# Kernel tuning notes

Hardware: AMD Instinct MI355X
Metric: run time of the kernel (lower is better)

The kernel has to match this reference:

```python
import jax, jax.numpy as jnp
import numpy as np

B, S, D = 4, 2048, 2048  # batch, seq, input_dim == state_dim
N = D

def setup_inputs() -> dict:
    key = jax.random.key(0)
    ks = jax.random.split(key, 6)
    x = jax.random.normal(ks[0], (B, S, D), dtype=jnp.float32)
    W_dt = jax.random.normal(ks[1], (N, D), dtype=jnp.float32) / np.sqrt(D)
    b_dt = jnp.ones((N,), dtype=jnp.float32)  # dt_proj.bias.fill_(1.0)
    W_B = jax.random.normal(ks[2], (N, D), dtype=jnp.float32) / np.sqrt(D)
    W_C = jax.random.normal(ks[3], (D, N), dtype=jnp.float32) / np.sqrt(N)
    A_log = jax.random.normal(ks[4], (N,), dtype=jnp.float32) * 0.5 - 1.0
    D_skip = jnp.zeros((D,), dtype=jnp.float32)
    return {"x": x, "W_dt": W_dt, "b_dt": b_dt, "W_B": W_B, "W_C": W_C,
            "A_log": A_log, "D_skip": D_skip}

def reference(x, W_dt, b_dt, W_B, W_C, A_log, D_skip):
    # dt = softplus(x @ W_dt^T + b_dt) -> [B,S,N]
    dt = jax.nn.softplus(jnp.einsum('bsd,nd->bsn', x, W_dt) + b_dt)
    Bp = jnp.einsum('bsd,nd->bsn', x, W_B)          # [B,S,N]
    A = -jnp.exp(A_log)                              # [N]
    A_bar = jnp.exp(dt * A)                          # [B,S,N]
    inputs = (dt * Bp) * x                           # B_bar * x (N == D)
    # selective scan: h_t = A_bar_t * h_{t-1} + inputs_t
    h0 = jnp.zeros((x.shape[0], A_log.shape[0]), dtype=x.dtype)
    def step(h, ab_u):
        ab, u = ab_u
        h = ab * h + u
        return h, h
    # scan over time axis: move S to leading axis
    _, h_all = jax.lax.scan(step, h0,
                            (jnp.swapaxes(A_bar, 0, 1), jnp.swapaxes(inputs, 0, 1)))
    h_all = jnp.swapaxes(h_all, 0, 1)                # [B,S,N]
    out = jnp.einsum('bsn,dn->bsd', h_all, W_C) + D_skip * x
    return out
```

## Files before the change

kernel.cpp:

```cpp
#include <hip/hip_runtime.h>

#define SEQ    2048
#define DIM    2048
#define NBATCH 4
#define MTOT   (NBATCH * SEQ)
#define CHUNKS 32
#define CLEN   (SEQ / CHUNKS)
#define NBM    (MTOT / 128)
#define TILE_E (128 * 32)

typedef __bf16 bf16_t;
typedef __bf16 bf16x8 __attribute__((ext_vector_type(8)));
typedef float  f32x4  __attribute__((ext_vector_type(4)));
typedef unsigned short u16x4 __attribute__((ext_vector_type(4)));

__device__ __forceinline__ unsigned short f2bf_rne(float f) {
    unsigned int u = __float_as_uint(f);
    u += 0x7fffu + ((u >> 16) & 1u);
    return (unsigned short)(u >> 16);
}

__global__ void k_convert(const float* __restrict__ src,
                          unsigned short* __restrict__ dst, int n4) {
    int i = blockIdx.x * blockDim.x + threadIdx.x;
    if (i >= n4) return;
    f32x4 v = ((const f32x4*)src)[i];
    u16x4 o;
    o[0] = f2bf_rne(v[0]); o[1] = f2bf_rne(v[1]);
    o[2] = f2bf_rne(v[2]); o[3] = f2bf_rne(v[3]);
    ((u16x4*)dst)[i] = o;
}

__global__ void k_convert_ilv(const float* __restrict__ src,
                              unsigned short* __restrict__ dst, int n4, int phase) {
    int i = blockIdx.x * blockDim.x + threadIdx.x;
    if (i >= n4) return;
    const int R4 = DIM / 4;
    int nrow = i / R4;
    int dcol = i - nrow * R4;
    f32x4 v = ((const f32x4*)src)[i];
    u16x4 o;
    o[0] = f2bf_rne(v[0]); o[1] = f2bf_rne(v[1]);
    o[2] = f2bf_rne(v[2]); o[3] = f2bf_rne(v[3]);
    ((u16x4*)dst)[(2 * nrow + phase) * R4 + dcol] = o;
}

__global__ void k_prep_a(const float* __restrict__ A_log, float* __restrict__ negA, int n) {
    int i = blockIdx.x * blockDim.x + threadIdx.x;
    if (i < n) negA[i] = -__expf(A_log[i]);
}

__device__ __forceinline__ void stage_tile(const bf16_t* __restrict__ g, long rowbase,
                                           int K, int k0, bf16_t* lds,
                                           int wave, int lane) {
    const int rl     = lane >> 2;
    const int gchunk = (lane & 3) ^ ((lane >> 3) & 3);
#pragma unroll
    for (int q = 0; q < 2; q++) {
        const bf16_t* ga = g + (rowbase + wave * 32 + q * 16 + rl) * (long)K
                             + k0 + gchunk * 8;
        __builtin_amdgcn_global_load_lds(
            (const __attribute__((address_space(1))) void*)ga,
            (__attribute__((address_space(3))) void*)((char*)lds + (wave * 32 + q * 16) * 64),
            16, 0, 0);
    }
}

template <int KITERS>
__device__ __forceinline__ void gemm_main(const bf16_t* __restrict__ A,
                                          const bf16_t* __restrict__ Bm,
                                          int K, long arow0, long brow0,
                                          bf16_t* As, bf16_t* Bs,
                                          f32x4 acc[4][4],
                                          int wave, int lane, int wm, int wn) {
    const int l15  = lane & 15;
    const int quad = lane >> 4;
    const int swz  = (quad ^ ((l15 >> 1) & 3)) * 8;

    stage_tile(A,  arow0, K, 0,  As,          wave, lane);
    stage_tile(Bm, brow0, K, 0,  Bs,          wave, lane);
    stage_tile(A,  arow0, K, 32, As + TILE_E, wave, lane);
    stage_tile(Bm, brow0, K, 32, Bs + TILE_E, wave, lane);

    int cur = 0;
    for (int i = 0; i < KITERS - 1; ++i) {
        asm volatile("s_waitcnt vmcnt(4)\n\ts_barrier" ::: "memory");
        const bf16_t* ap = As + cur * TILE_E;
        const bf16_t* bp = Bs + cur * TILE_E;
        bf16x8 af[4], bfr[4];
#pragma unroll
        for (int t = 0; t < 4; t++) {
            af[t]  = *(const bf16x8*)(ap + (wm * 64 + t * 16 + l15) * 32 + swz);
            bfr[t] = *(const bf16x8*)(bp + (wn * 64 + t * 16 + l15) * 32 + swz);
        }
        if (i + 2 < KITERS) {
            int nxt = cur + 2; if (nxt >= 3) nxt -= 3;
            stage_tile(A,  arow0, K, (i + 2) * 32, As + nxt * TILE_E, wave, lane);
            stage_tile(Bm, brow0, K, (i + 2) * 32, Bs + nxt * TILE_E, wave, lane);
        }
#pragma unroll
        for (int t = 0; t < 4; t++)
#pragma unroll
            for (int j = 0; j < 4; j++)
                acc[t][j] = __builtin_amdgcn_mfma_f32_16x16x32_bf16(
                    af[t], bfr[j], acc[t][j], 0, 0, 0);
        cur += 1; if (cur == 3) cur = 0;
    }
    asm volatile("s_waitcnt vmcnt(0)\n\ts_barrier" ::: "memory");
    const bf16_t* ap = As + cur * TILE_E;
    const bf16_t* bp = Bs + cur * TILE_E;
    bf16x8 af[4], bfr[4];
#pragma unroll
    for (int t = 0; t < 4; t++) {
        af[t]  = *(const bf16x8*)(ap + (wm * 64 + t * 16 + l15) * 32 + swz);
        bfr[t] = *(const bf16x8*)(bp + (wn * 64 + t * 16 + l15) * 32 + swz);
    }
#pragma unroll
    for (int t = 0; t < 4; t++)
#pragma unroll
        for (int j = 0; j < 4; j++)
            acc[t][j] = __builtin_amdgcn_mfma_f32_16x16x32_bf16(
                af[t], bfr[j], acc[t][j], 0, 0, 0);
}

__global__ __launch_bounds__(256)
void k_gemm_fused(const bf16_t* __restrict__ A, const bf16_t* __restrict__ Wcat,
                  const float* __restrict__ x, const float* __restrict__ b_dt,
                  const float* __restrict__ negA,
                  float* __restrict__ abuf, float* __restrict__ ubuf) {
    __shared__ __align__(16) bf16_t As[3 * TILE_E];
    __shared__ __align__(16) bf16_t Bs[3 * TILE_E];

    const int tid  = threadIdx.x;
    const int lane = tid & 63;
    const int wave = tid >> 6;
    const int wm   = wave >> 1;
    const int wn   = wave & 1;
    int flat = blockIdx.y * gridDim.x + blockIdx.x;
    int bm = flat % NBM;
    int bn = flat / NBM;

    f32x4 acc[4][4];
#pragma unroll
    for (int i = 0; i < 4; i++)
#pragma unroll
        for (int j = 0; j < 4; j++) acc[i][j] = (f32x4){0.f, 0.f, 0.f, 0.f};

    gemm_main<DIM / 32>(A, Wcat, DIM, (long)bm * 128, (long)bn * 128,
                        As, Bs, acc, wave, lane, wm, wn);

    const int l15  = lane & 15;
    const int quad = lane >> 4;
    const int odd  = l15 & 1;
#pragma unroll
    for (int i = 0; i < 4; i++) {
#pragma unroll
        for (int j = 0; j < 4; j++) {
#pragma unroll
            for (int r = 0; r < 4; r++) {
                float v = acc[i][j][r];
                float w = __shfl_xor(v, 1);
                float dtpre = odd ? w : v;
                float bpv   = odd ? v : w;
                long row = (long)bm * 128 + wm * 64 + i * 16 + quad * 4 + r;
                int  col = bn * 128 + wn * 64 + j * 16 + l15;
                int  n   = col >> 1;
                float z  = dtpre + b_dt[n];
                float dt = (z > 15.f) ? z : __logf(1.f + __expf(z));
                float a  = __expf(negA[n] * dt);
                float u  = dt * bpv * x[row * DIM + n];
                long idx = row * DIM + n;
                if (odd) ubuf[idx] = u; else abuf[idx] = a;
            }
        }
    }
}

__global__ __launch_bounds__(256)
void k_gemm_bt(const bf16_t* __restrict__ A, const bf16_t* __restrict__ Bm,
               float* __restrict__ C, int N, int K,
               const float* __restrict__ skip, const float* __restrict__ xres) {
    __shared__ __align__(16) bf16_t As[3 * TILE_E];
    __shared__ __align__(16) bf16_t Bs[3 * TILE_E];

    const int tid  = threadIdx.x;
    const int lane = tid & 63;
    const int wave = tid >> 6;
    const int wm   = wave >> 1;
    const int wn   = wave & 1;
    int flat = blockIdx.y * gridDim.x + blockIdx.x;
    int bm = flat % NBM;
    int bn = flat / NBM;

    f32x4 acc[4][4];
#pragma unroll
    for (int i = 0; i < 4; i++)
#pragma unroll
        for (int j = 0; j < 4; j++) acc[i][j] = (f32x4){0.f, 0.f, 0.f, 0.f};

    gemm_main<DIM / 32>(A, Bm, K, (long)bm * 128, (long)bn * 128,
                        As, Bs, acc, wave, lane, wm, wn);

    const int l15  = lane & 15;
    const int quad = lane >> 4;
#pragma unroll
    for (int i = 0; i < 4; i++) {
#pragma unroll
        for (int j = 0; j < 4; j++) {
#pragma unroll
            for (int r = 0; r < 4; r++) {
                long row = (long)bm * 128 + wm * 64 + i * 16 + quad * 4 + r;
                long col = (long)bn * 128 + wn * 64 + j * 16 + l15;
                long idx = row * (long)N + col;
                float v = acc[i][j][r];
                if (skip) v += skip[col] * xres[idx];
                C[idx] = v;
            }
        }
    }
}

__global__ void k_scan1(const float* __restrict__ a, const float* __restrict__ u,
                        float* __restrict__ P, float* __restrict__ V) {
    int t = blockIdx.x * blockDim.x + threadIdx.x;
    int n = t & (DIM - 1);
    int c = (t >> 11) & (CHUNKS - 1);
    int b = t >> 16;
    long base = ((long)b * SEQ + (long)c * CLEN) * DIM + n;
    float p = 1.f, v = 0.f;
    for (int s = 0; s < CLEN; s++) {
        float av = a[base + (long)s * DIM];
        float uv = u[base + (long)s * DIM];
        v = av * v + uv;
        p *= av;
    }
    P[t] = p; V[t] = v;
}

__global__ void k_scan2(const float* __restrict__ P, const float* __restrict__ V,
                        float* __restrict__ carry) {
    int t = blockIdx.x * blockDim.x + threadIdx.x;
    int n = t & (DIM - 1);
    int b = t >> 11;
    float H = 0.f;
    for (int c = 0; c < CHUNKS; c++) {
        long idx = ((long)b * CHUNKS + c) * DIM + n;
        carry[idx] = H;
        H = P[idx] * H + V[idx];
    }
}

__global__ void k_scan3(const float* __restrict__ a, const float* __restrict__ u,
                        const float* __restrict__ carry,
                        unsigned short* __restrict__ h) {
    int t = blockIdx.x * blockDim.x + threadIdx.x;
    int n = t & (DIM - 1);
    int c = (t >> 11) & (CHUNKS - 1);
    int b = t >> 16;
    long base = ((long)b * SEQ + (long)c * CLEN) * DIM + n;
    float H = carry[t];
    for (int s = 0; s < CLEN; s++) {
        float av = a[base + (long)s * DIM];
        float uv = u[base + (long)s * DIM];
        H = av * H + uv;
        h[base + (long)s * DIM] = f2bf_rne(H);
    }
}

extern "C" void kernel_launch(void* const* d_in, const int* in_sizes, int n_in,
                              void* d_out, int out_size, void* d_ws, size_t ws_size,
                              hipStream_t stream) {
    const float* x      = (const float*)d_in[0];
    const float* W_dt   = (const float*)d_in[1];
    const float* b_dt   = (const float*)d_in[2];
    const float* W_B    = (const float*)d_in[3];
    const float* W_C    = (const float*)d_in[4];
    const float* A_log  = (const float*)d_in[5];
    const float* D_skip = (const float*)d_in[6];
    float* out = (float*)d_out;

    char* ws = (char*)d_ws;
    size_t off = 0;
    auto alloc = [&](size_t bytes) -> char* {
        char* p = ws + off;
        off += (bytes + 255) & ~(size_t)255;
        return p;
    };
    unsigned short* xb   = (unsigned short*)alloc((size_t)MTOT * DIM * 2);
    unsigned short* wcat = (unsigned short*)alloc((size_t)2 * DIM * DIM * 2);
    unsigned short* wcb  = (unsigned short*)alloc((size_t)DIM * DIM * 2);
    float* abuf  = (float*)alloc((size_t)MTOT * DIM * 4);
    float* ubuf  = (float*)alloc((size_t)MTOT * DIM * 4);
    float* P     = (float*)alloc((size_t)NBATCH * CHUNKS * DIM * 4);
    float* V     = (float*)alloc((size_t)NBATCH * CHUNKS * DIM * 4);
    float* carry = (float*)alloc((size_t)NBATCH * CHUNKS * DIM * 4);
    float* negA  = (float*)alloc((size_t)DIM * 4);

    const int n4x = MTOT * DIM / 4;
    const int n4w = DIM * DIM / 4;
    k_convert<<<n4x / 256, 256, 0, stream>>>(x, xb, n4x);
    k_convert_ilv<<<n4w / 256, 256, 0, stream>>>(W_dt, wcat, n4w, 0);
    k_convert_ilv<<<n4w / 256, 256, 0, stream>>>(W_B,  wcat, n4w, 1);
    k_convert<<<n4w / 256, 256, 0, stream>>>(W_C, wcb, n4w);
    k_prep_a<<<DIM / 256, 256, 0, stream>>>(A_log, negA, DIM);

    dim3 fgrid(2 * DIM / 128, MTOT / 128);
    k_gemm_fused<<<fgrid, 256, 0, stream>>>((const bf16_t*)xb, (const bf16_t*)wcat,
                                            x, b_dt, negA, abuf, ubuf);

    const int scan_threads = NBATCH * CHUNKS * DIM;
    k_scan1<<<scan_threads / 256, 256, 0, stream>>>(abuf, ubuf, P, V);
    k_scan2<<<(NBATCH * DIM) / 256, 256, 0, stream>>>(P, V, carry);
    k_scan3<<<scan_threads / 256, 256, 0, stream>>>(abuf, ubuf, carry, xb );

    dim3 ggrid(DIM / 128, MTOT / 128);
    k_gemm_bt<<<ggrid, 256, 0, stream>>>((const bf16_t*)xb, (const bf16_t*)wcb,
                                         out, DIM, DIM, D_skip, x);
}
```

Measured before the change: 604.7 us.

## Store scan intermediates in bf16 and double-buffer GEMM staging

The A_bar and input buffers written by the fused GEMM epilogue are now stored as bf16 instead of fp32, halving the traffic through the two scan passes that read them. The scan kernels now process two channels per thread with packed loads and stores. The GEMM main loop also drops from triple to double buffering with a full vmcnt(0) wait each iteration, which reduces LDS use but exposes more load latency. Rounding A_bar to bf16 before it is multiplied across many time steps risks accuracy drift.

```diff
diff --git a/kernel.cpp b/kernel.cpp
--- a/kernel.cpp
+++ b/kernel.cpp
@@ -13,11 +13,15 @@
 typedef __bf16 bf16x8 __attribute__((ext_vector_type(8)));
 typedef float  f32x4  __attribute__((ext_vector_type(4)));
 typedef unsigned short u16x4 __attribute__((ext_vector_type(4)));
+typedef unsigned short u16x2 __attribute__((ext_vector_type(2)));
 
 __device__ __forceinline__ unsigned short f2bf_rne(float f) {
     unsigned int u = __float_as_uint(f);
     u += 0x7fffu + ((u >> 16) & 1u);
     return (unsigned short)(u >> 16);
+}
+__device__ __forceinline__ float bf2f(unsigned short v) {
+    return __uint_as_float((unsigned int)v << 16);
 }
 
 __global__ void k_convert(const float* __restrict__ src,
@@ -77,26 +81,22 @@
     const int quad = lane >> 4;
     const int swz  = (quad ^ ((l15 >> 1) & 3)) * 8;
 
-    stage_tile(A,  arow0, K, 0,  As,          wave, lane);
-    stage_tile(Bm, brow0, K, 0,  Bs,          wave, lane);
-    stage_tile(A,  arow0, K, 32, As + TILE_E, wave, lane);
-    stage_tile(Bm, brow0, K, 32, Bs + TILE_E, wave, lane);
-
-    int cur = 0;
-    for (int i = 0; i < KITERS - 1; ++i) {
-        asm volatile("s_waitcnt vmcnt(4)\n\ts_barrier" ::: "memory");
-        const bf16_t* ap = As + cur * TILE_E;
-        const bf16_t* bp = Bs + cur * TILE_E;
+    stage_tile(A,  arow0, K, 0, As, wave, lane);
+    stage_tile(Bm, brow0, K, 0, Bs, wave, lane);
+
+    for (int i = 0; i < KITERS; ++i) {
+        asm volatile("s_waitcnt vmcnt(0)\n\ts_barrier" ::: "memory");
+        const bf16_t* ap = As + (i & 1) * TILE_E;
+        const bf16_t* bp = Bs + (i & 1) * TILE_E;
         bf16x8 af[4], bfr[4];
 #pragma unroll
         for (int t = 0; t < 4; t++) {
             af[t]  = *(const bf16x8*)(ap + (wm * 64 + t * 16 + l15) * 32 + swz);
             bfr[t] = *(const bf16x8*)(bp + (wn * 64 + t * 16 + l15) * 32 + swz);
         }
-        if (i + 2 < KITERS) {
-            int nxt = cur + 2; if (nxt >= 3) nxt -= 3;
-            stage_tile(A,  arow0, K, (i + 2) * 32, As + nxt * TILE_E, wave, lane);
-            stage_tile(Bm, brow0, K, (i + 2) * 32, Bs + nxt * TILE_E, wave, lane);
+        if (i + 1 < KITERS) {
+            stage_tile(A,  arow0, K, (i + 1) * 32, As + ((i + 1) & 1) * TILE_E, wave, lane);
+            stage_tile(Bm, brow0, K, (i + 1) * 32, Bs + ((i + 1) & 1) * TILE_E, wave, lane);
         }
 #pragma unroll
         for (int t = 0; t < 4; t++)
@@ -104,32 +104,16 @@
             for (int j = 0; j < 4; j++)
                 acc[t][j] = __builtin_amdgcn_mfma_f32_16x16x32_bf16(
                     af[t], bfr[j], acc[t][j], 0, 0, 0);
-        cur += 1; if (cur == 3) cur = 0;
-    }
-    asm volatile("s_waitcnt vmcnt(0)\n\ts_barrier" ::: "memory");
-    const bf16_t* ap = As + cur * TILE_E;
-    const bf16_t* bp = Bs + cur * TILE_E;
-    bf16x8 af[4], bfr[4];
-#pragma unroll
-    for (int t = 0; t < 4; t++) {
-        af[t]  = *(const bf16x8*)(ap + (wm * 64 + t * 16 + l15) * 32 + swz);
-        bfr[t] = *(const bf16x8*)(bp + (wn * 64 + t * 16 + l15) * 32 + swz);
-    }
-#pragma unroll
-    for (int t = 0; t < 4; t++)
-#pragma unroll
-        for (int j = 0; j < 4; j++)
-            acc[t][j] = __builtin_amdgcn_mfma_f32_16x16x32_bf16(
-                af[t], bfr[j], acc[t][j], 0, 0, 0);
+    }
 }
 
 __global__ __launch_bounds__(256)
 void k_gemm_fused(const bf16_t* __restrict__ A, const bf16_t* __restrict__ Wcat,
                   const float* __restrict__ x, const float* __restrict__ b_dt,
                   const float* __restrict__ negA,
-                  float* __restrict__ abuf, float* __restrict__ ubuf) {
-    __shared__ __align__(16) bf16_t As[3 * TILE_E];
-    __shared__ __align__(16) bf16_t Bs[3 * TILE_E];
+                  unsigned short* __restrict__ abuf, unsigned short* __restrict__ ubuf) {
+    __shared__ __align__(16) bf16_t As[2 * TILE_E];
+    __shared__ __align__(16) bf16_t Bs[2 * TILE_E];
 
     const int tid  = threadIdx.x;
     const int lane = tid & 63;
@@ -170,7 +154,7 @@
                 float a  = __expf(negA[n] * dt);
                 float u  = dt * bpv * x[row * DIM + n];
                 long idx = row * DIM + n;
-                if (odd) ubuf[idx] = u; else abuf[idx] = a;
+                if (odd) ubuf[idx] = f2bf_rne(u); else abuf[idx] = f2bf_rne(a);
             }
         }
     }
@@ -180,8 +164,8 @@
 void k_gemm_bt(const bf16_t* __restrict__ A, const bf16_t* __restrict__ Bm,
                float* __restrict__ C, int N, int K,
                const float* __restrict__ skip, const float* __restrict__ xres) {
-    __shared__ __align__(16) bf16_t As[3 * TILE_E];
-    __shared__ __align__(16) bf16_t Bs[3 * TILE_E];
+    __shared__ __align__(16) bf16_t As[2 * TILE_E];
+    __shared__ __align__(16) bf16_t Bs[2 * TILE_E];
 
     const int tid  = threadIdx.x;
     const int lane = tid & 63;
@@ -220,21 +204,25 @@
     }
 }
 
-__global__ void k_scan1(const float* __restrict__ a, const float* __restrict__ u,
+__global__ void k_scan1(const unsigned short* __restrict__ a,
+                        const unsigned short* __restrict__ u,
                         float* __restrict__ P, float* __restrict__ V) {
-    int t = blockIdx.x * blockDim.x + threadIdx.x;
-    int n = t & (DIM - 1);
-    int c = (t >> 11) & (CHUNKS - 1);
-    int b = t >> 16;
-    long base = ((long)b * SEQ + (long)c * CLEN) * DIM + n;
-    float p = 1.f, v = 0.f;
+    int t  = blockIdx.x * blockDim.x + threadIdx.x;
+    int n2 = t & (DIM / 2 - 1);
+    int c  = (t >> 10) & (CHUNKS - 1);
+    int b  = t >> 15;
+    long base = ((long)b * SEQ + (long)c * CLEN) * DIM + n2 * 2;
+    float p0 = 1.f, v0 = 0.f, p1 = 1.f, v1 = 0.f;
     for (int s = 0; s < CLEN; s++) {
-        float av = a[base + (long)s * DIM];
-        float uv = u[base + (long)s * DIM];
-        v = av * v + uv;
-        p *= av;
-    }
-    P[t] = p; V[t] = v;
+        u16x2 av = *(const u16x2*)(a + base + (long)s * DIM);
+        u16x2 uv = *(const u16x2*)(u + base + (long)s * DIM);
+        float a0 = bf2f(av[0]), a1 = bf2f(av[1]);
+        v0 = a0 * v0 + bf2f(uv[0]);  p0 *= a0;
+        v1 = a1 * v1 + bf2f(uv[1]);  p1 *= a1;
+    }
+    long pidx = ((long)b * CHUNKS + c) * DIM + n2 * 2;
+    *(float2*)(P + pidx) = make_float2(p0, p1);
+    *(float2*)(V + pidx) = make_float2(v0, v1);
 }
 
 __global__ void k_scan2(const float* __restrict__ P, const float* __restrict__ V,
@@ -250,20 +238,25 @@
     }
 }
 
-__global__ void k_scan3(const float* __restrict__ a, const float* __restrict__ u,
+__global__ void k_scan3(const unsigned short* __restrict__ a,
+                        const unsigned short* __restrict__ u,
                         const float* __restrict__ carry,
                         unsigned short* __restrict__ h) {
-    int t = blockIdx.x * blockDim.x + threadIdx.x;
-    int n = t & (DIM - 1);
-    int c = (t >> 11) & (CHUNKS - 1);
-    int b = t >> 16;
-    long base = ((long)b * SEQ + (long)c * CLEN) * DIM + n;
-    float H = carry[t];
+    int t  = blockIdx.x * blockDim.x + threadIdx.x;
+    int n2 = t & (DIM / 2 - 1);
+    int c  = (t >> 10) & (CHUNKS - 1);
+    int b  = t >> 15;
+    long base = ((long)b * SEQ + (long)c * CLEN) * DIM + n2 * 2;
+    long cidx = ((long)b * CHUNKS + c) * DIM + n2 * 2;
+    float2 Hc = *(const float2*)(carry + cidx);
+    float H0 = Hc.x, H1 = Hc.y;
     for (int s = 0; s < CLEN; s++) {
-        float av = a[base + (long)s * DIM];
-        float uv = u[base + (long)s * DIM];
-        H = av * H + uv;
-        h[base + (long)s * DIM] = f2bf_rne(H);
+        u16x2 av = *(const u16x2*)(a + base + (long)s * DIM);
+        u16x2 uv = *(const u16x2*)(u + base + (long)s * DIM);
+        H0 = bf2f(av[0]) * H0 + bf2f(uv[0]);
+        H1 = bf2f(av[1]) * H1 + bf2f(uv[1]);
+        u16x2 o; o[0] = f2bf_rne(H0); o[1] = f2bf_rne(H1);
+        *(u16x2*)(h + base + (long)s * DIM) = o;
     }
 }
 
@@ -289,8 +282,8 @@
     unsigned short* xb   = (unsigned short*)alloc((size_t)MTOT * DIM * 2);
     unsigned short* wcat = (unsigned short*)alloc((size_t)2 * DIM * DIM * 2);
     unsigned short* wcb  = (unsigned short*)alloc((size_t)DIM * DIM * 2);
-    float* abuf  = (float*)alloc((size_t)MTOT * DIM * 4);
-    float* ubuf  = (float*)alloc((size_t)MTOT * DIM * 4);
+    unsigned short* abuf = (unsigned short*)alloc((size_t)MTOT * DIM * 2);
+    unsigned short* ubuf = (unsigned short*)alloc((size_t)MTOT * DIM * 2);
     float* P     = (float*)alloc((size_t)NBATCH * CHUNKS * DIM * 4);
     float* V     = (float*)alloc((size_t)NBATCH * CHUNKS * DIM * 4);
     float* carry = (float*)alloc((size_t)NBATCH * CHUNKS * DIM * 4);
@@ -308,10 +301,10 @@
     k_gemm_fused<<<fgrid, 256, 0, stream>>>((const bf16_t*)xb, (const bf16_t*)wcat,
                                             x, b_dt, negA, abuf, ubuf);
 
-    const int scan_threads = NBATCH * CHUNKS * DIM;
-    k_scan1<<<scan_threads / 256, 256, 0, stream>>>(abuf, ubuf, P, V);
+    const int scan2_threads = NBATCH * CHUNKS * DIM / 2;
+    k_scan1<<<scan2_threads / 256, 256, 0, stream>>>(abuf, ubuf, P, V);
     k_scan2<<<(NBATCH * DIM) / 256, 256, 0, stream>>>(P, V, carry);
-    k_scan3<<<scan_threads / 256, 256, 0, stream>>>(abuf, ubuf, carry, xb );
+    k_scan3<<<scan2_threads / 256, 256, 0, stream>>>(abuf, ubuf, carry, xb );
 
     dim3 ggrid(DIM / 128, MTOT / 128);
     k_gemm_bt<<<ggrid, 256, 0, stream>>>((const bf16_t*)xb, (const bf16_t*)wcb,
```

Measured after the change: 561.7 us. -7.1%, faster.
